# Performance work log

Hardware: AMD Instinct MI355X
Metric: run time of the kernel (lower is better)

## Reference

```python
import jax, jax.numpy as jnp
import numpy as np

D_MODEL = 256
N_HEAD = 8
D_FF = 2048
BATCH = 4
TOK_PER_BATCH = 4096
N = BATCH * TOK_PER_BATCH  # 16384 total queries == total keys
L = 32  # neighbors per query
EPS = 1e-5


def _layer_norm(x, g, b):
    mu = jnp.mean(x, axis=-1, keepdims=True)
    var = jnp.mean(jnp.square(x - mu), axis=-1, keepdims=True)
    return (x - mu) * jax.lax.rsqrt(var + EPS) * g + b


def setup_inputs() -> dict:
    key = jax.random.key(0)
    ks = jax.random.split(key, 16)
    d, f = D_MODEL, D_FF
    s = 1.0 / np.sqrt(d)
    inp = {
        "src": jax.random.normal(ks[0], (N, d), dtype=jnp.float32),
        "index_pair": jax.random.randint(ks[1], (N, L), 0, TOK_PER_BATCH, dtype=jnp.int64),
        "query_batch_cnt": jnp.full((BATCH,), TOK_PER_BATCH, dtype=jnp.int32),
        "key_batch_cnt": jnp.full((BATCH,), TOK_PER_BATCH, dtype=jnp.int32),
        "index_pair_batch": jnp.repeat(jnp.arange(BATCH, dtype=jnp.int32), TOK_PER_BATCH),
        "Wq": jax.random.normal(ks[2], (d, d), dtype=jnp.float32) * s,
        "bq": jnp.zeros((d,), jnp.float32),
        "Wk": jax.random.normal(ks[3], (d, d), dtype=jnp.float32) * s,
        "bk": jnp.zeros((d,), jnp.float32),
        "Wv": jax.random.normal(ks[4], (d, d), dtype=jnp.float32) * s,
        "bv": jnp.zeros((d,), jnp.float32),
        "Wo": jax.random.normal(ks[5], (d, d), dtype=jnp.float32) * s,
        "bo": jnp.zeros((d,), jnp.float32),
        "W1": jax.random.normal(ks[6], (d, f), dtype=jnp.float32) * s,
        "b1": jnp.zeros((f,), jnp.float32),
        "W2": jax.random.normal(ks[7], (f, d), dtype=jnp.float32) * (1.0 / np.sqrt(f)),
        "b2": jnp.zeros((d,), jnp.float32),
        "g1": jnp.ones((d,), jnp.float32),
        "be1": jnp.zeros((d,), jnp.float32),
        "g2": jnp.ones((d,), jnp.float32),
        "be2": jnp.zeros((d,), jnp.float32),
    }
    return inp


def _attention(src, index_pair, key_batch_cnt, index_pair_batch,
               Wq, bq, Wk, bk, Wv, bv, Wo, bo):
    n, d = src.shape
    hd = d // N_HEAD
    scale = hd ** -0.5
    q = (src @ Wq + bq).reshape(n, N_HEAD, hd) * scale
    k = src @ Wk + bk
    v = src @ Wv + bv
    # exclusive cumsum -> start offset of each batch's key segment
    key_start = jnp.cumsum(key_batch_cnt) - key_batch_cnt          # [B]
    offs = key_start[index_pair_batch]                             # [N]
    valid = index_pair >= 0                                        # [N, L]
    idx = jnp.where(valid, index_pair + offs[:, None].astype(index_pair.dtype), 0)
    kg = k[idx].reshape(n, L, N_HEAD, hd)                          # gathered keys
    vg = v[idx].reshape(n, L, N_HEAD, hd)                          # gathered values
    logits = jnp.einsum("nhd,nlhd->nhl", q, kg)
    logits = jnp.where(valid[:, None, :], logits, jnp.float32(-1e9))
    attn = jax.nn.softmax(logits, axis=-1)
    out = jnp.einsum("nhl,nlhd->nhd", attn, vg).reshape(n, d)
    return out @ Wo + bo


def reference(src, index_pair, query_batch_cnt, key_batch_cnt, index_pair_batch,
              Wq, bq, Wk, bk, Wv, bv, Wo, bo, W1, b1, W2, b2, g1, be1, g2, be2):
    src2 = _attention(src, index_pair, key_batch_cnt, index_pair_batch,
                      Wq, bq, Wk, bk, Wv, bv, Wo, bo)
    x = _layer_norm(src + src2, g1, be1)
    ff = jax.nn.relu(x @ W1 + b1) @ W2 + b2
    return _layer_norm(x + ff, g2, be2)
```

## Files before the change

### kernel.cpp

```cpp
#include <hip/hip_runtime.h>
#include <hip/hip_bf16.h>
#include <cstddef>
#include <cstdint>

#define D_MODEL 256
#define N_TOK   16384
#define NHEAD   8
#define HDIM    32
#define LNEIGH  32
#define DFF     2048

#define SMEM_LN (16384 + 65536 + 2048 + 2048 + 256 + 256)

typedef short bf16x8 __attribute__((ext_vector_type(8)));
typedef float f32x4  __attribute__((ext_vector_type(4)));

__device__ __forceinline__ float b2f(short s) {
    unsigned u = ((unsigned)(unsigned short)s) << 16;
    return __builtin_bit_cast(float, u);
}

__device__ __forceinline__ void gload_lds16(const void* g, void* l) {
    auto* gp = reinterpret_cast<const __attribute__((address_space(1))) uint32_t*>(
        reinterpret_cast<uintptr_t>(g));
    auto* lp = reinterpret_cast<__attribute__((address_space(3))) uint32_t*>(
        reinterpret_cast<uintptr_t>(l));
    __builtin_amdgcn_global_load_lds(gp, lp, 16, 0, 0);
}

__global__ __launch_bounds__(256) void gemm_bt(
    const __hip_bfloat16* __restrict__ A, int lda,
    const __hip_bfloat16* __restrict__ Bt, int ldb,
    const float* __restrict__ bias,
    __hip_bfloat16* __restrict__ outb, int ldc,
    int M, int N, int K, int relu)
{
    __shared__ short Asm[2][128 * 32];
    __shared__ short Bsm[2][128 * 32];

    const int tid  = threadIdx.x;
    const int lane = tid & 63;
    const int wid  = tid >> 6;
    const int wr   = wid >> 1;
    const int wc   = wid & 1;
    const int bm   = blockIdx.y * 128;
    const int bn   = blockIdx.x * 128;

    f32x4 acc[4][4] = {};
    const int srow = lane >> 2;
    const int seg  = (lane & 3) * 8;

    auto stage = [&](int buf, int k0) {
        #pragma unroll
        for (int t = 0; t < 2; ++t) {
            int rbase = wid * 32 + t * 16;
            gload_lds16(A  + (size_t)(bm + rbase + srow) * lda + k0 + seg, &Asm[buf][rbase * 32]);
            gload_lds16(Bt + (size_t)(bn + rbase + srow) * ldb + k0 + seg, &Bsm[buf][rbase * 32]);
        }
    };

    const int nk = K >> 5;
    stage(0, 0);
    __syncthreads();

    for (int kk = 0; kk < nk; ++kk) {
        const int cur = kk & 1;
        if (kk + 1 < nk) stage(cur ^ 1, (kk + 1) << 5);

        bf16x8 a[4], b[4];
        #pragma unroll
        for (int i = 0; i < 4; ++i)
            a[i] = *(const bf16x8*)&Asm[cur][(wr * 64 + i * 16 + (lane & 15)) * 32 + (lane >> 4) * 8];
        #pragma unroll
        for (int j = 0; j < 4; ++j)
            b[j] = *(const bf16x8*)&Bsm[cur][(wc * 64 + j * 16 + (lane & 15)) * 32 + (lane >> 4) * 8];
        #pragma unroll
        for (int i = 0; i < 4; ++i)
            #pragma unroll
            for (int j = 0; j < 4; ++j)
                acc[i][j] = __builtin_amdgcn_mfma_f32_16x16x32_bf16(a[i], b[j], acc[i][j], 0, 0, 0);
        __syncthreads();
    }

    #pragma unroll
    for (int i = 0; i < 4; ++i) {
        int rbase = bm + wr * 64 + i * 16 + ((lane >> 4) << 2);
        #pragma unroll
        for (int j = 0; j < 4; ++j) {
            int col = bn + wc * 64 + j * 16 + (lane & 15);
            float bval = bias ? bias[col] : 0.0f;
            #pragma unroll
            for (int r = 0; r < 4; ++r) {
                int row = rbase + r;
                float v = acc[i][j][r] + bval;
                if (relu) v = fmaxf(v, 0.0f);
                outb[(size_t)row * ldc + col] = __float2bfloat16(v);
            }
        }
    }
}

__global__ __launch_bounds__(512) void gemm_bk64_ln(
    const __hip_bfloat16* __restrict__ A, int lda,
    const __hip_bfloat16* __restrict__ Bt, int ldb,
    const float* __restrict__ bias,
    const float* __restrict__ residf,
    const __hip_bfloat16* __restrict__ residb,
    const float* __restrict__ g,
    const float* __restrict__ be,
    float* __restrict__ outf,
    __hip_bfloat16* __restrict__ outb,
    int K)
{
    extern __shared__ char smem[];
    short* AsmB = (short*)smem;
    short* BsmB = (short*)(smem + 16384);
    float* lnS  = (float*)(smem + 81920);
    float* lnS2 = (float*)(smem + 83968);
    float* rmu  = (float*)(smem + 86016);
    float* rrs  = (float*)(smem + 86272);

    const int tid  = threadIdx.x;
    const int lane = tid & 63;
    const int wid  = tid >> 6;
    const int wr   = wid >> 2;
    const int wc   = wid & 3;
    const int bm   = blockIdx.x * 64;
    const int lo   = lane & 15;
    const int hi   = lane >> 4;

    f32x4 acc[2][4] = {};

    const int srow8 = lane >> 3;
    const int sc    = lane & 7;
    const int ssw   = ((sc ^ srow8) << 3);

    auto stage = [&](int buf, int k0) {
        gload_lds16(A + (size_t)(bm + wid * 8 + srow8) * lda + k0 + ssw,
                    AsmB + buf * 4096 + (wid * 8) * 64);
        #pragma unroll
        for (int t = 0; t < 4; ++t) {
            int rb = wid * 32 + t * 8;
            gload_lds16(Bt + (size_t)(rb + srow8) * ldb + k0 + ssw,
                        BsmB + buf * 16384 + rb * 64);
        }
    };

    const int nk = K >> 6;
    stage(0, 0);
    __syncthreads();

    for (int kk = 0; kk < nk; ++kk) {
        const int cur = kk & 1;
        if (kk + 1 < nk) stage(cur ^ 1, (kk + 1) << 6);

        const short* Ab = AsmB + cur * 4096;
        const short* Bb = BsmB + cur * 16384;
        #pragma unroll
        for (int ks = 0; ks < 2; ++ks) {
            const int csw = ((ks * 4 + hi) ^ (lo & 7)) << 3;
            bf16x8 a[2], b[4];
            #pragma unroll
            for (int i = 0; i < 2; ++i)
                a[i] = *(const bf16x8*)&Ab[(wr * 32 + i * 16 + lo) * 64 + csw];
            #pragma unroll
            for (int j = 0; j < 4; ++j)
                b[j] = *(const bf16x8*)&Bb[(wc * 64 + j * 16 + lo) * 64 + csw];
            #pragma unroll
            for (int i = 0; i < 2; ++i)
                #pragma unroll
                for (int j = 0; j < 4; ++j)
                    acc[i][j] = __builtin_amdgcn_mfma_f32_16x16x32_bf16(a[i], b[j], acc[i][j], 0, 0, 0);
        }
        __syncthreads();
    }

    float ps[2][4] = {}, ps2[2][4] = {};
    #pragma unroll
    for (int j = 0; j < 4; ++j) {
        int col = wc * 64 + j * 16 + lo;
        float bval = bias ? bias[col] : 0.0f;
        #pragma unroll
        for (int i = 0; i < 2; ++i) {
            #pragma unroll
            for (int r = 0; r < 4; ++r) {
                int row = bm + wr * 32 + i * 16 + hi * 4 + r;
                float v = acc[i][j][r] + bval;
                size_t o = (size_t)row * 256 + col;
                if (residf) v += residf[o];
                if (residb) v += __bfloat162float(residb[o]);
                acc[i][j][r] = v;
                ps[i][r]  += v;
                ps2[i][r] += v * v;
            }
        }
    }
    #pragma unroll
    for (int i = 0; i < 2; ++i)
        #pragma unroll
        for (int r = 0; r < 4; ++r) {
            #pragma unroll
            for (int m = 1; m < 16; m <<= 1) {
                ps[i][r]  += __shfl_xor(ps[i][r],  m);
                ps2[i][r] += __shfl_xor(ps2[i][r], m);
            }
        }
    if (lo == 0) {
        #pragma unroll
        for (int i = 0; i < 2; ++i)
            #pragma unroll
            for (int r = 0; r < 4; ++r) {
                int rl = wr * 32 + i * 16 + hi * 4 + r;
                lnS[wid * 64 + rl]  = ps[i][r];
                lnS2[wid * 64 + rl] = ps2[i][r];
            }
    }
    __syncthreads();
    if (tid < 64) {
        int base = (tid >> 5) * 4;
        float s  = lnS[base * 64 + tid] + lnS[(base + 1) * 64 + tid]
                 + lnS[(base + 2) * 64 + tid] + lnS[(base + 3) * 64 + tid];
        float s2 = lnS2[base * 64 + tid] + lnS2[(base + 1) * 64 + tid]
                 + lnS2[(base + 2) * 64 + tid] + lnS2[(base + 3) * 64 + tid];
        float mu  = s * (1.0f / 256.0f);
        float var = s2 * (1.0f / 256.0f) - mu * mu;
        rmu[tid] = mu;
        rrs[tid] = rsqrtf(var + 1e-5f);
    }
    __syncthreads();

    #pragma unroll
    for (int j = 0; j < 4; ++j) {
        int col = wc * 64 + j * 16 + lo;
        float gg = g[col], bb = be[col];
        #pragma unroll
        for (int i = 0; i < 2; ++i) {
            #pragma unroll
            for (int r = 0; r < 4; ++r) {
                int rl = wr * 32 + i * 16 + hi * 4 + r;
                float v = (acc[i][j][r] - rmu[rl]) * rrs[rl] * gg + bb;
                size_t o = (size_t)(bm + rl) * 256 + col;
                if (outf) outf[o] = v;
                if (outb) outb[o] = __float2bfloat16(v);
            }
        }
    }
}

__global__ __launch_bounds__(256) void gemm_qkv(
    const __hip_bfloat16* __restrict__ A,
    const __hip_bfloat16* __restrict__ Bt,
    const float* __restrict__ bias,
    float* __restrict__ qf,
    __hip_bfloat16* __restrict__ kvb)
{
    __shared__ short Asm[2][128 * 32];
    __shared__ short Bsm[2][128 * 32];

    const int tid  = threadIdx.x;
    const int lane = tid & 63;
    const int wid  = tid >> 6;
    const int wr   = wid >> 1;
    const int wc   = wid & 1;
    const int bm   = blockIdx.y * 128;
    const int bn   = blockIdx.x * 128;

    f32x4 acc[4][4] = {};
    const int srow = lane >> 2;
    const int seg  = (lane & 3) * 8;

    auto stage = [&](int buf, int k0) {
        #pragma unroll
        for (int t = 0; t < 2; ++t) {
            int rbase = wid * 32 + t * 16;
            gload_lds16(A  + (size_t)(bm + rbase + srow) * 256 + k0 + seg, &Asm[buf][rbase * 32]);
            gload_lds16(Bt + (size_t)(bn + rbase + srow) * 256 + k0 + seg, &Bsm[buf][rbase * 32]);
        }
    };

    stage(0, 0);
    __syncthreads();
    for (int kk = 0; kk < 8; ++kk) {
        const int cur = kk & 1;
        if (kk + 1 < 8) stage(cur ^ 1, (kk + 1) << 5);
        bf16x8 a[4], b[4];
        #pragma unroll
        for (int i = 0; i < 4; ++i)
            a[i] = *(const bf16x8*)&Asm[cur][(wr * 64 + i * 16 + (lane & 15)) * 32 + (lane >> 4) * 8];
        #pragma unroll
        for (int j = 0; j < 4; ++j)
            b[j] = *(const bf16x8*)&Bsm[cur][(wc * 64 + j * 16 + (lane & 15)) * 32 + (lane >> 4) * 8];
        #pragma unroll
        for (int i = 0; i < 4; ++i)
            #pragma unroll
            for (int j = 0; j < 4; ++j)
                acc[i][j] = __builtin_amdgcn_mfma_f32_16x16x32_bf16(a[i], b[j], acc[i][j], 0, 0, 0);
        __syncthreads();
    }

    const bool isq = (bn < 256);
    #pragma unroll
    for (int i = 0; i < 4; ++i) {
        int rbase = bm + wr * 64 + i * 16 + ((lane >> 4) << 2);
        #pragma unroll
        for (int j = 0; j < 4; ++j) {
            int col = bn + wc * 64 + j * 16 + (lane & 15);
            float bval = bias[col];
            #pragma unroll
            for (int r = 0; r < 4; ++r) {
                int row = rbase + r;
                float v = acc[i][j][r] + bval;
                if (isq) qf[(size_t)row * 256 + col] = v;
                else     kvb[(size_t)row * 512 + (col - 256)] = __float2bfloat16(v);
            }
        }
    }
}

__global__ __launch_bounds__(256) void cvt_f2b(
    const float* __restrict__ x, __hip_bfloat16* __restrict__ y, int n)
{
    int i = (blockIdx.x * 256 + threadIdx.x) * 4;
    if (i >= n) return;
    float4 v = *(const float4*)(x + i);
    y[i + 0] = __float2bfloat16(v.x);
    y[i + 1] = __float2bfloat16(v.y);
    y[i + 2] = __float2bfloat16(v.z);
    y[i + 3] = __float2bfloat16(v.w);
}

__global__ __launch_bounds__(256) void cvt_wt_tiled(
    const float* __restrict__ W, __hip_bfloat16* __restrict__ Wt,
    int K, int N, int ldo, float scale)
{
    __shared__ float t[32][33];
    const int n0 = blockIdx.x * 32;
    const int k0 = blockIdx.y * 32;
    const int tx = threadIdx.x & 31;
    const int ty = threadIdx.x >> 5;
    #pragma unroll
    for (int i = 0; i < 32; i += 8)
        t[ty + i][tx] = W[(size_t)(k0 + ty + i) * N + n0 + tx];
    __syncthreads();
    #pragma unroll
    for (int i = 0; i < 32; i += 8)
        Wt[(size_t)(n0 + ty + i) * ldo + k0 + tx] = __float2bfloat16(t[tx][ty + i] * scale);
}

__global__ __launch_bounds__(256) void cvt_w3_tiled(
    const float* __restrict__ Wa, const float* __restrict__ Wb,
    const float* __restrict__ Wc, __hip_bfloat16* __restrict__ Wt,
    float scale_a)
{
    __shared__ float t[32][33];
    const int n0 = blockIdx.x * 32;
    const int k0 = blockIdx.y * 32;
    const float* W = (n0 < 256) ? Wa : (n0 < 512 ? Wb : Wc);
    const float sc = (n0 < 256) ? scale_a : 1.0f;
    const int ncol = n0 & 255;
    const int tx = threadIdx.x & 31;
    const int ty = threadIdx.x >> 5;
    #pragma unroll
    for (int i = 0; i < 32; i += 8)
        t[ty + i][tx] = W[(size_t)(k0 + ty + i) * 256 + ncol + tx];
    __syncthreads();
    #pragma unroll
    for (int i = 0; i < 32; i += 8)
        Wt[(size_t)(n0 + ty + i) * 256 + k0 + tx] = __float2bfloat16(t[tx][ty + i] * sc);
}

__global__ __launch_bounds__(768) void make_bqkv(
    const float* __restrict__ bq, const float* __restrict__ bk,
    const float* __restrict__ bv, const int* __restrict__ kbc, int nb,
    float* __restrict__ o, int* __restrict__ ks, float qs)
{
    int i = threadIdx.x;
    if (i < 256)      o[i] = bq[i] * qs;
    else if (i < 512) o[i] = bk[i - 256];
    else              o[i] = bv[i - 512];
    if (i < nb) {
        int acc = 0;
        for (int j = 0; j < i; ++j) acc += kbc[j];
        ks[i] = acc;
    }
}

__global__ __launch_bounds__(256) void attn_wave(
    const float* __restrict__ qf,
    const __hip_bfloat16* __restrict__ kvb,
    const int* __restrict__ index_pair,
    const int* __restrict__ ipb,
    const int* __restrict__ key_start,
    __hip_bfloat16* __restrict__ out)
{
    const int w    = threadIdx.x >> 6;
    const int lane = threadIdx.x & 63;
    const int bid  = blockIdx.x;
    const int n  = (bid & 7) * 2048 + (bid >> 3) * 4 + w;
    const int c  = lane & 31;
    const int pp = lane >> 5;

    int raw = index_pair[(size_t)n * LNEIGH + c];
    int ks  = key_start[ipb[n]];
    int gi0 = (raw >= 0) ? raw + ks : -1;

    const float* qp = qf + (size_t)n * 256 + c * 8;
    float4 q0 = *(const float4*)(qp);
    float4 q1 = *(const float4*)(qp + 4);

    int gi[16];
    #pragma unroll
    for (int i = 0; i < 16; ++i) gi[i] = __shfl(gi0, 2 * i + pp);

    bf16x8 kr[16];
    #pragma unroll
    for (int i = 0; i < 16; ++i) {
        int g = gi[i] < 0 ? 0 : gi[i];
        kr[i] = *(const bf16x8*)(kvb + (size_t)g * 512 + c * 8);
    }

    float s[16];
    #pragma unroll
    for (int i = 0; i < 16; ++i) {
        float t = q0.x * b2f(kr[i][0]) + q0.y * b2f(kr[i][1])
                + q0.z * b2f(kr[i][2]) + q0.w * b2f(kr[i][3])
                + q1.x * b2f(kr[i][4]) + q1.y * b2f(kr[i][5])
                + q1.z * b2f(kr[i][6]) + q1.w * b2f(kr[i][7]);
        t += __shfl_xor(t, 1);
        t += __shfl_xor(t, 2);
        s[i] = (gi[i] < 0) ? -1e9f : t;
    }

    bf16x8 vr[16];
    #pragma unroll
    for (int i = 0; i < 16; ++i) {
        int g = gi[i] < 0 ? 0 : gi[i];
        vr[i] = *(const bf16x8*)(kvb + (size_t)g * 512 + 256 + c * 8);
    }

    float m = s[0];
    #pragma unroll
    for (int i = 1; i < 16; ++i) m = fmaxf(m, s[i]);
    m = fmaxf(m, __shfl_xor(m, 32));
    float tot = 0.0f;
    #pragma unroll
    for (int i = 0; i < 16; ++i) { s[i] = __expf(s[i] - m); tot += s[i]; }
    tot += __shfl_xor(tot, 32);
    const float inv = 1.0f / tot;

    float a[8] = {};
    #pragma unroll
    for (int i = 0; i < 16; ++i) {
        float wt = s[i] * inv;
        #pragma unroll
        for (int j = 0; j < 8; ++j) a[j] += wt * b2f(vr[i][j]);
    }
    #pragma unroll
    for (int j = 0; j < 8; ++j) a[j] += __shfl_xor(a[j], 32);

    if (pp == 0) {
        bf16x8 ov;
        #pragma unroll
        for (int j = 0; j < 8; ++j)
            ov[j] = __builtin_bit_cast(short, __float2bfloat16(a[j]));
        *(bf16x8*)((short*)out + (size_t)n * 256 + c * 8) = ov;
    }
}

extern "C" void kernel_launch(void* const* d_in, const int* in_sizes, int n_in,
                              void* d_out, int out_size, void* d_ws, size_t ws_size,
                              hipStream_t stream)
{
    const float* src = (const float*)d_in[0];
    const int*   index_pair = (const int*)d_in[1];
    const int*   kbc = (const int*)d_in[3];
    const int*   ipb = (const int*)d_in[4];
    const float* Wq = (const float*)d_in[5];
    const float* bq = (const float*)d_in[6];
    const float* Wk = (const float*)d_in[7];
    const float* bk = (const float*)d_in[8];
    const float* Wv = (const float*)d_in[9];
    const float* bv = (const float*)d_in[10];
    const float* Wo = (const float*)d_in[11];
    const float* bo = (const float*)d_in[12];
    const float* W1 = (const float*)d_in[13];
    const float* b1 = (const float*)d_in[14];
    const float* W2 = (const float*)d_in[15];
    const float* b2 = (const float*)d_in[16];
    const float* g1 = (const float*)d_in[17];
    const float* be1 = (const float*)d_in[18];
    const float* g2 = (const float*)d_in[19];
    const float* be2 = (const float*)d_in[20];
    float* out = (float*)d_out;
    const int nb = in_sizes[3];

    char* ws = (char*)d_ws;
    const size_t O_SRCBF = 0;
    const size_t O_QF    = 8388608;
    const size_t O_KVB   = 25165824;
    const size_t O_ATTN  = 41943040;
    const size_t O_HC    = 0;
    const size_t O_XBF   = 67108864;
    const size_t O_WQKV  = 75497472;
    const size_t O_WO    = O_WQKV + 768 * 256 * 2;
    const size_t O_W1    = O_WO + 256 * 256 * 2;
    const size_t O_W2    = O_W1 + (size_t)DFF * 256 * 2;
    const size_t O_BQKV  = O_W2 + (size_t)DFF * 256 * 2;
    const size_t O_KS    = O_BQKV + 768 * 4;

    __hip_bfloat16* src_bf  = (__hip_bfloat16*)(ws + O_SRCBF);
    float*          qf      = (float*)(ws + O_QF);
    __hip_bfloat16* kvb     = (__hip_bfloat16*)(ws + O_KVB);
    __hip_bfloat16* attn_bf = (__hip_bfloat16*)(ws + O_ATTN);
    __hip_bfloat16* hc      = (__hip_bfloat16*)(ws + O_HC);
    __hip_bfloat16* x_bf    = (__hip_bfloat16*)(ws + O_XBF);
    __hip_bfloat16* WqkvT   = (__hip_bfloat16*)(ws + O_WQKV);
    __hip_bfloat16* WoT     = (__hip_bfloat16*)(ws + O_WO);
    __hip_bfloat16* W1T     = (__hip_bfloat16*)(ws + O_W1);
    __hip_bfloat16* W2T     = (__hip_bfloat16*)(ws + O_W2);
    float*          bqkv    = (float*)(ws + O_BQKV);
    int*            ksbuf   = (int*)(ws + O_KS);

    const dim3 blk(256);
    const float qscale = 0.17677669529663687f;

    hipFuncSetAttribute(reinterpret_cast<const void*>(gemm_bk64_ln),
                        hipFuncAttributeMaxDynamicSharedMemorySize, SMEM_LN);

    cvt_f2b<<<N_TOK * D_MODEL / 4 / 256, blk, 0, stream>>>(src, src_bf, N_TOK * D_MODEL);
    cvt_w3_tiled<<<dim3(24, 8), blk, 0, stream>>>(Wq, Wk, Wv, WqkvT, qscale);
    cvt_wt_tiled<<<dim3(8, 8),  blk, 0, stream>>>(Wo, WoT, 256, 256, 256, 1.0f);
    cvt_wt_tiled<<<dim3(64, 8), blk, 0, stream>>>(W1, W1T, 256, DFF, 256, 1.0f);
    cvt_wt_tiled<<<dim3(8, 64), blk, 0, stream>>>(W2, W2T, DFF, 256, DFF, 1.0f);
    make_bqkv<<<1, 768, 0, stream>>>(bq, bk, bv, kbc, nb, bqkv, ksbuf, qscale);

    gemm_qkv<<<dim3(6, 128), blk, 0, stream>>>(src_bf, WqkvT, bqkv, qf, kvb);

    attn_wave<<<dim3(N_TOK / 4), blk, 0, stream>>>(qf, kvb, index_pair, ipb, ksbuf, attn_bf);

    gemm_bk64_ln<<<dim3(N_TOK / 64), dim3(512), SMEM_LN, stream>>>(
        attn_bf, 256, WoT, 256, bo, src, nullptr, g1, be1,
        nullptr, x_bf, 256);

    gemm_bt<<<dim3(16, 128), blk, 0, stream>>>(
        x_bf, 256, W1T, 256, b1, hc, DFF, N_TOK, DFF, 256, 1);

    gemm_bk64_ln<<<dim3(N_TOK / 64), dim3(512), SMEM_LN, stream>>>(
        hc, DFF, W2T, DFF, b2, nullptr, x_bf, g2, be2,
        out, nullptr, DFF);
}
```

Before: 159.9 us.

## Load B operand directly into registers and triple-buffer A in LDS for LN GEMM

```diff
diff --git a/kernel.cpp b/kernel.cpp
--- a/kernel.cpp
+++ b/kernel.cpp
@@ -9,8 +9,6 @@
 #define HDIM    32
 #define LNEIGH  32
 #define DFF     2048
-
-#define SMEM_LN (16384 + 65536 + 2048 + 2048 + 256 + 256)
 
 typedef short bf16x8 __attribute__((ext_vector_type(8)));
 typedef float f32x4  __attribute__((ext_vector_type(4)));
@@ -100,7 +98,7 @@
     }
 }
 
-__global__ __launch_bounds__(512) void gemm_bk64_ln(
+__global__ __launch_bounds__(512) void gemm_breg_ln(
     const __hip_bfloat16* __restrict__ A, int lda,
     const __hip_bfloat16* __restrict__ Bt, int ldb,
     const float* __restrict__ bias,
@@ -112,13 +110,9 @@
     __hip_bfloat16* __restrict__ outb,
     int K)
 {
-    extern __shared__ char smem[];
-    short* AsmB = (short*)smem;
-    short* BsmB = (short*)(smem + 16384);
-    float* lnS  = (float*)(smem + 81920);
-    float* lnS2 = (float*)(smem + 83968);
-    float* rmu  = (float*)(smem + 86016);
-    float* rrs  = (float*)(smem + 86272);
+    __shared__ short AsmB[3][64 * 64];
+    __shared__ float lnS[8][64], lnS2[8][64];
+    __shared__ float rmu[64], rrs[64];
 
     const int tid  = threadIdx.x;
     const int lane = tid & 63;
@@ -135,44 +129,67 @@
     const int sc    = lane & 7;
     const int ssw   = ((sc ^ srow8) << 3);
 
-    auto stage = [&](int buf, int k0) {
+    auto stageA = [&](int buf, int k0) {
         gload_lds16(A + (size_t)(bm + wid * 8 + srow8) * lda + k0 + ssw,
-                    AsmB + buf * 4096 + (wid * 8) * 64);
-        #pragma unroll
-        for (int t = 0; t < 4; ++t) {
-            int rb = wid * 32 + t * 8;
-            gload_lds16(Bt + (size_t)(rb + srow8) * ldb + k0 + ssw,
-                        BsmB + buf * 16384 + rb * 64);
-        }
+                    &AsmB[buf][(wid * 8) * 64]);
     };
 
+    const __hip_bfloat16* brow[4];
+    #pragma unroll
+    for (int j = 0; j < 4; ++j)
+        brow[j] = Bt + (size_t)(wc * 64 + j * 16 + lo) * ldb + hi * 8;
+
+    bf16x8 bcur[4][2], bnext[4][2];
     const int nk = K >> 6;
-    stage(0, 0);
-    __syncthreads();
+
+    stageA(0, 0);
+    stageA(1, 64);
+    #pragma unroll
+    for (int j = 0; j < 4; ++j)
+        #pragma unroll
+        for (int ks = 0; ks < 2; ++ks)
+            bcur[j][ks] = *(const bf16x8*)(brow[j] + ks * 32);
+    asm volatile("s_waitcnt vmcnt(9)" ::: "memory");
+    __builtin_amdgcn_s_barrier();
+    __builtin_amdgcn_sched_barrier(0);
 
     for (int kk = 0; kk < nk; ++kk) {
-        const int cur = kk & 1;
-        if (kk + 1 < nk) stage(cur ^ 1, (kk + 1) << 6);
-
-        const short* Ab = AsmB + cur * 4096;
-        const short* Bb = BsmB + cur * 16384;
+        const int cur = kk % 3;
+        if (kk + 2 < nk) stageA((kk + 2) % 3, (kk + 2) << 6);
+        if (kk + 1 < nk) {
+            #pragma unroll
+            for (int j = 0; j < 4; ++j)
+                #pragma unroll
+                for (int ks = 0; ks < 2; ++ks)
+                    bnext[j][ks] = *(const bf16x8*)(brow[j] + (size_t)(kk + 1) * 64 + ks * 32);
+        }
+
+        const short* Ab = &AsmB[cur][0];
         #pragma unroll
         for (int ks = 0; ks < 2; ++ks) {
             const int csw = ((ks * 4 + hi) ^ (lo & 7)) << 3;
-            bf16x8 a[2], b[4];
-            #pragma unroll
-            for (int i = 0; i < 2; ++i)
-                a[i] = *(const bf16x8*)&Ab[(wr * 32 + i * 16 + lo) * 64 + csw];
-            #pragma unroll
-            for (int j = 0; j < 4; ++j)
-                b[j] = *(const bf16x8*)&Bb[(wc * 64 + j * 16 + lo) * 64 + csw];
-            #pragma unroll
-            for (int i = 0; i < 2; ++i)
-                #pragma unroll
-                for (int j = 0; j < 4; ++j)
-                    acc[i][j] = __builtin_amdgcn_mfma_f32_16x16x32_bf16(a[i], b[j], acc[i][j], 0, 0, 0);
-        }
-        __syncthreads();
+            bf16x8 a0 = *(const bf16x8*)&Ab[(wr * 32 + lo) * 64 + csw];
+            bf16x8 a1 = *(const bf16x8*)&Ab[(wr * 32 + 16 + lo) * 64 + csw];
+            acc[0][0] = __builtin_amdgcn_mfma_f32_16x16x32_bf16(a0, bcur[0][ks], acc[0][0], 0, 0, 0);
+            acc[0][1] = __builtin_amdgcn_mfma_f32_16x16x32_bf16(a0, bcur[1][ks], acc[0][1], 0, 0, 0);
+            acc[0][2] = __builtin_amdgcn_mfma_f32_16x16x32_bf16(a0, bcur[2][ks], acc[0][2], 0, 0, 0);
+            acc[0][3] = __builtin_amdgcn_mfma_f32_16x16x32_bf16(a0, bcur[3][ks], acc[0][3], 0, 0, 0);
+            acc[1][0] = __builtin_amdgcn_mfma_f32_16x16x32_bf16(a1, bcur[0][ks], acc[1][0], 0, 0, 0);
+            acc[1][1] = __builtin_amdgcn_mfma_f32_16x16x32_bf16(a1, bcur[1][ks], acc[1][1], 0, 0, 0);
+            acc[1][2] = __builtin_amdgcn_mfma_f32_16x16x32_bf16(a1, bcur[2][ks], acc[1][2], 0, 0, 0);
+            acc[1][3] = __builtin_amdgcn_mfma_f32_16x16x32_bf16(a1, bcur[3][ks], acc[1][3], 0, 0, 0);
+        }
+        #pragma unroll
+        for (int j = 0; j < 4; ++j)
+            #pragma unroll
+            for (int ks = 0; ks < 2; ++ks)
+                bcur[j][ks] = bnext[j][ks];
+
+        if (kk + 2 < nk)      asm volatile("s_waitcnt vmcnt(9)" ::: "memory");
+        else if (kk + 1 < nk) asm volatile("s_waitcnt vmcnt(8)" ::: "memory");
+        else                  asm volatile("s_waitcnt vmcnt(0)" ::: "memory");
+        __builtin_amdgcn_s_barrier();
+        __builtin_amdgcn_sched_barrier(0);
     }
 
     float ps[2][4] = {}, ps2[2][4] = {};
@@ -211,17 +228,15 @@
             #pragma unroll
             for (int r = 0; r < 4; ++r) {
                 int rl = wr * 32 + i * 16 + hi * 4 + r;
-                lnS[wid * 64 + rl]  = ps[i][r];
-                lnS2[wid * 64 + rl] = ps2[i][r];
+                lnS[wid][rl]  = ps[i][r];
+                lnS2[wid][rl] = ps2[i][r];
             }
     }
     __syncthreads();
     if (tid < 64) {
         int base = (tid >> 5) * 4;
-        float s  = lnS[base * 64 + tid] + lnS[(base + 1) * 64 + tid]
-                 + lnS[(base + 2) * 64 + tid] + lnS[(base + 3) * 64 + tid];
-        float s2 = lnS2[base * 64 + tid] + lnS2[(base + 1) * 64 + tid]
-                 + lnS2[(base + 2) * 64 + tid] + lnS2[(base + 3) * 64 + tid];
+        float s  = lnS[base][tid] + lnS[base + 1][tid] + lnS[base + 2][tid] + lnS[base + 3][tid];
+        float s2 = lnS2[base][tid] + lnS2[base + 1][tid] + lnS2[base + 2][tid] + lnS2[base + 3][tid];
         float mu  = s * (1.0f / 256.0f);
         float var = s2 * (1.0f / 256.0f) - mu * mu;
         rmu[tid] = mu;
@@ -524,9 +539,6 @@
     const dim3 blk(256);
     const float qscale = 0.17677669529663687f;
 
-    hipFuncSetAttribute(reinterpret_cast<const void*>(gemm_bk64_ln),
-                        hipFuncAttributeMaxDynamicSharedMemorySize, SMEM_LN);
-
     cvt_f2b<<<N_TOK * D_MODEL / 4 / 256, blk, 0, stream>>>(src, src_bf, N_TOK * D_MODEL);
     cvt_w3_tiled<<<dim3(24, 8), blk, 0, stream>>>(Wq, Wk, Wv, WqkvT, qscale);
     cvt_wt_tiled<<<dim3(8, 8),  blk, 0, stream>>>(Wo, WoT, 256, 256, 256, 1.0f);
@@ -538,14 +550,14 @@
 
     attn_wave<<<dim3(N_TOK / 4), blk, 0, stream>>>(qf, kvb, index_pair, ipb, ksbuf, attn_bf);
 
-    gemm_bk64_ln<<<dim3(N_TOK / 64), dim3(512), SMEM_LN, stream>>>(
+    gemm_breg_ln<<<dim3(N_TOK / 64), dim3(512), 0, stream>>>(
         attn_bf, 256, WoT, 256, bo, src, nullptr, g1, be1,
         nullptr, x_bf, 256);
 
     gemm_bt<<<dim3(16, 128), blk, 0, stream>>>(
         x_bf, 256, W1T, 256, b1, hc, DFF, N_TOK, DFF, 256, 1);
 
-    gemm_bk64_ln<<<dim3(N_TOK / 64), dim3(512), SMEM_LN, stream>>>(
+    gemm_breg_ln<<<dim3(N_TOK / 64), dim3(512), 0, stream>>>(
         hc, DFF, W2T, DFF, b2, nullptr, x_bf, g2, be2,
         out, nullptr, DFF);
 }
```

New measurement: 213.4 us. +33.5%, slower.
